# Performance work log

Measured on AMD Instinct MI355X. Metric: run time of the kernel, lower is better.

## Reference

```python
import jax, jax.numpy as jnp
import numpy as np

B, L, C, H, W = 2, 32, 128, 32, 32
R_MIN, R_MAX = 0.8, 0.99


def setup_inputs() -> dict:
    key = jax.random.key(0)
    ks = jax.random.split(key, 12)
    x = jax.random.normal(ks[0], (B, L, C, H, W), jnp.float32)
    # LRU initialization exactly as in the torch module
    u1 = jax.random.uniform(ks[1], (C, H), jnp.float32)
    u2 = jax.random.uniform(ks[2], (C, H), jnp.float32)
    nu_log = jnp.log(-0.5 * jnp.log(u1 * (R_MAX**2 - R_MIN**2) + R_MIN**2))
    theta_log = jnp.log(u2 * 2.0 * jnp.pi)
    abs_lam = jnp.exp(-jnp.exp(nu_log))  # |lambda| = exp(-nu)
    gamma_log = jnp.log(jnp.sqrt(1.0 - abs_lam**2))
    params_log = jnp.concatenate([nu_log, theta_log, gamma_log], axis=0)  # [3C, H]
    s = 0.05
    Wb_re = jax.random.normal(ks[3], (C, C), jnp.float32) * s
    Wb_im = jax.random.normal(ks[4], (C, C), jnp.float32) * s
    bb_re = jax.random.normal(ks[5], (C,), jnp.float32) * s
    bb_im = jax.random.normal(ks[6], (C,), jnp.float32) * s
    Wc_re = jax.random.normal(ks[7], (C, C), jnp.float32) * s
    Wc_im = jax.random.normal(ks[8], (C, C), jnp.float32) * s
    bc_re = jax.random.normal(ks[9], (C,), jnp.float32) * s
    bc_im = jax.random.normal(ks[10], (C,), jnp.float32) * s
    ln_w = jnp.ones((C, H, W), jnp.float32)
    ln_b = jnp.zeros((C, H, W), jnp.float32)
    return dict(x=x, params_log=params_log, Wb_re=Wb_re, Wb_im=Wb_im, bb_re=bb_re,
                bb_im=bb_im, Wc_re=Wc_re, Wc_im=Wc_im, bc_re=bc_re, bc_im=bc_im,
                ln_w=ln_w, ln_b=ln_b)


def reference(x, params_log, Wb_re, Wb_im, bb_re, bb_im, Wc_re, Wc_im, bc_re, bc_im, ln_w, ln_b):
    Cn = x.shape[2]
    nu = jnp.exp(params_log[:Cn])           # [C,H]
    theta = jnpp_exp = jnp.exp(params_log[Cn:2 * Cn])
    gamma = jnp.exp(params_log[2 * Cn:])    # [C,H]
    lam = jnp.exp(-nu + 1j * theta)         # [C,H] complex, |lam|<1

    # FFT2 over spatial dims
    h = jnp.fft.fft2(x.astype(jnp.complex64))  # [B,L,C,H,W]
    # complex 1x1 conv proj_B (CxC GEMM per pixel)
    Wb = (Wb_re + 1j * Wb_im).astype(jnp.complex64)
    bb = (bb_re + 1j * bb_im).astype(jnp.complex64)
    h = jnp.einsum('oc,blchw->blohw', Wb, h) + bb[None, None, :, None, None]
    # gamma gating, broadcast over B,L,W
    h = h * gamma[None, None, :, :, None]

    # linear recurrence y_t = lam * y_{t-1} + h_t (pscan), lam constant in t
    lam_b = lam[None, :, :, None]  # [1,C,H,1] broadcasts over [B,C,H,W]
    def step(carry, ht):
        y = lam_b * carry + ht
        return y, y
    h_t = jnp.moveaxis(h, 1, 0)  # [L,B,C,H,W]
    _, ys = jax.lax.scan(step, jnp.zeros_like(h_t[0]), h_t)
    h = jnp.moveaxis(ys, 0, 1)   # [B,L,C,H,W]
    last_hidden_out = h[:, -1:]

    h = jnp.fft.ifft2(h)
    Wc = (Wc_re + 1j * Wc_im).astype(jnp.complex64)
    bc = (bc_re + 1j * bc_im).astype(jnp.complex64)
    h = jnp.einsum('oc,blchw->blohw', Wc, h) + bc[None, None, :, None, None]
    h = h.real  # real cast, dropout is identity in eval

    # LayerNorm over (C,H,W) jointly
    mean = jnp.mean(h, axis=(2, 3, 4), keepdims=True)
    var = jnp.var(h, axis=(2, 3, 4), keepdims=True)
    h = (h - mean) / jnp.sqrt(var + 1e-5) * ln_w + ln_b
    return h + x, last_hidden_out
```

## Files before the change

kernel.cpp:

```cpp
#include <hip/hip_runtime.h>
#include <cstdint>
#include <cstddef>

#define DEVINL __device__ __forceinline__

static constexpr int Bdim = 2, Ldim = 32, Cdim = 128, Hdim = 32, Wdim = 32;
static constexpr int HW  = Hdim * Wdim;
static constexpr int CHW = Cdim * HW;
static constexpr size_t OUT0_ELEMS = (size_t)Bdim * Ldim * CHW;
static constexpr size_t OUT1_CPLX  = (size_t)Bdim * CHW;

typedef __attribute__((ext_vector_type(8))) short short8v;
typedef __attribute__((ext_vector_type(4))) float f32x4;

DEVINL int bitrev5(int v) {
    return ((v&1)<<4) | ((v&2)<<2) | (v&4) | ((v&8)>>2) | ((v&16)>>4);
}
DEVINL unsigned short f2bf(float v) {
    unsigned u = __float_as_uint(v);
    return (unsigned short)((u + 0x7FFFu + ((u >> 16) & 1u)) >> 16);
}
DEVINL void bfsplit(float v, short& hi, short& lo) {
    unsigned short hb = f2bf(v);
    hi = (short)hb;
    float hf = __uint_as_float(((unsigned)hb) << 16);
    lo = (short)f2bf(v - hf);
}
DEVINL unsigned pack2bf(float2 v) {
    return (unsigned)f2bf(v.x) | ((unsigned)f2bf(v.y) << 16);
}
DEVINL float2 unpack2bf(unsigned u) {
    return make_float2(__uint_as_float(u << 16), __uint_as_float(u & 0xFFFF0000u));
}

template<int INV>
DEVINL void fft32_reg(float2 v[32]) {
    constexpr float TC[16] = { 1.0f, 0.980785280f, 0.923879533f, 0.831469612f,
                               0.707106781f, 0.555570233f, 0.382683432f, 0.195090322f,
                               0.0f, -0.195090322f, -0.382683432f, -0.555570233f,
                              -0.707106781f, -0.831469612f, -0.923879533f, -0.980785280f };
    constexpr float TS[16] = { 0.0f, -0.195090322f, -0.382683432f, -0.555570233f,
                              -0.707106781f, -0.831469612f, -0.923879533f, -0.980785280f,
                              -1.0f, -0.980785280f, -0.923879533f, -0.831469612f,
                              -0.707106781f, -0.555570233f, -0.382683432f, -0.195090322f };
#pragma unroll
    for (int st = 0; st < 5; ++st) {
        const int half = 1 << st;
#pragma unroll
        for (int bf = 0; bf < 16; ++bf) {
            const int g = bf >> st;
            const int j = bf & (half - 1);
            const int i0 = (g << (st+1)) + j;
            const float wr = TC[j << (4-st)];
            const float wi = INV ? -TS[j << (4-st)] : TS[j << (4-st)];
            float2 a0 = v[i0], a1 = v[i0+half];
            float tr = wr*a1.x - wi*a1.y;
            float ti = wr*a1.y + wi*a1.x;
            v[i0]      = make_float2(a0.x+tr, a0.y+ti);
            v[i0+half] = make_float2(a0.x-tr, a0.y-ti);
        }
    }
}

__global__ __launch_bounds__(256) void fft_h_fwd_bf_kernel(const float* __restrict__ x,
                                                           unsigned* __restrict__ Hf) {
    const int gid = blockIdx.x*256 + threadIdx.x;
    const int w = gid & 31;
    const size_t slice = (size_t)(gid >> 5);
    const float* src = x + slice*HW + w;
    float2 v[32];
#pragma unroll
    for (int i = 0; i < 32; ++i)
        v[i] = make_float2(src[(size_t)bitrev5(i)*Wdim], 0.f);
    fft32_reg<0>(v);
    unsigned* dst = Hf + slice*HW + w;
#pragma unroll
    for (int h = 0; h < 32; ++h) dst[(size_t)h*Wdim] = pack2bf(v[h]);
}

__global__ __launch_bounds__(256) void ifft_h_bf_kernel(const unsigned* __restrict__ Sin,
                                                        unsigned* __restrict__ Ysp) {
    const int gid = blockIdx.x*256 + threadIdx.x;
    const int w = gid & 31;
    const size_t slice = (size_t)(gid >> 5);
    const unsigned* src = Sin + slice*HW + w;
    float2 v[32];
#pragma unroll
    for (int i = 0; i < 32; ++i)
        v[i] = unpack2bf(src[(size_t)bitrev5(i)*Wdim]);
    fft32_reg<1>(v);
    const float sc = 1.0f / 32.0f;
    unsigned* dst = Ysp + slice*HW + w;
#pragma unroll
    for (int h = 0; h < 32; ++h)
        dst[(size_t)h*Wdim] = pack2bf(make_float2(v[h].x*sc, v[h].y*sc));
}

__global__ __launch_bounds__(256) void pack_w_kernel(
    const float* __restrict__ Wb_re, const float* __restrict__ Wb_im,
    const float* __restrict__ Wc_re, const float* __restrict__ Wc_im,
    short* __restrict__ Apack)
{
    const int gid = blockIdx.x*256 + threadIdx.x;
    const int a    = gid >> 12;
    const int rem  = gid & 4095;
    const int f    = rem >> 6;
    const int lane = rem & 63;
    const int m  = f >> 3, kc = f & 7;
    const int row = m*16 + (lane & 15);
    const int kbase = kc*32 + ((lane >> 4) << 3);
    short8v hi8, lo8;
#pragma unroll
    for (int j = 0; j < 8; ++j) {
        const int k = kbase + j;
        const int half = k >> 7;
        const int c = k & 127;
        float v;
        if (a == 0)      v = half ? -Wb_im[row*Cdim + c] : Wb_re[row*Cdim + c];
        else if (a == 1) v = half ?  Wb_re[row*Cdim + c] : Wb_im[row*Cdim + c];
        else             v = half ? -Wc_im[row*Cdim + c] : Wc_re[row*Cdim + c];
        short h, l; bfsplit(v, h, l);
        hi8[j] = h; lo8[j] = l;
    }
    const size_t off = (size_t)(f*64 + lane)*8;
    *reinterpret_cast<short8v*>(Apack + (size_t)(2*a)  *32768 + off) = hi8;
    *reinterpret_cast<short8v*>(Apack + (size_t)(2*a+1)*32768 + off) = lo8;
}

template<int MODE>
__global__ __launch_bounds__(256) void mix_mfma3_kernel(
    const unsigned* __restrict__ Yin,
    unsigned* __restrict__ Sout,
    const short* __restrict__ Apack,
    const float* __restrict__ bre, const float* __restrict__ bim,
    const float* __restrict__ pl,
    unsigned short* __restrict__ outr,
    float2* __restrict__ lnpart)
{
    __shared__ short Bs[8][4][64][8];
    const int bx = blockIdx.x;
    const int bl = bx >> 4, tt = bx & 15;
    const int t = threadIdx.x;
    const int wv = t >> 6, lane = t & 63;

    const unsigned* src = Yin + (size_t)bl*CHW + tt*64;
#pragma unroll
    for (int g = 0; g < 4; ++g) {
        const int id = g*256 + t;
        const int hw = id & 63;
        const int co = id >> 6;
        const int kc = co >> 2;
        const int ln = (co & 3)*16 + (hw & 15);
        const int nt4 = hw >> 4;
        unsigned u[8];
#pragma unroll
        for (int j = 0; j < 8; ++j)
            u[j] = src[(size_t)(co*8 + j)*HW + hw];
        unsigned re[4], im[4];
#pragma unroll
        for (int p = 0; p < 4; ++p) {
            re[p] = (u[2*p] & 0xFFFFu) | (u[2*p+1] << 16);
            im[p] = (u[2*p] >> 16) | (u[2*p+1] & 0xFFFF0000u);
        }
        *reinterpret_cast<uint4*>(&Bs[kc][nt4][ln][0])   = make_uint4(re[0], re[1], re[2], re[3]);
        *reinterpret_cast<uint4*>(&Bs[kc+4][nt4][ln][0]) = make_uint4(im[0], im[1], im[2], im[3]);
    }
    __syncthreads();

    f32x4 accRe[2][4];
    f32x4 accIm[2][4];
#pragma unroll
    for (int mi = 0; mi < 2; ++mi)
#pragma unroll
        for (int nt = 0; nt < 4; ++nt) {
            accRe[mi][nt] = (f32x4)(0.0f);
            accIm[mi][nt] = (f32x4)(0.0f);
        }

    const short* Are_hi = Apack + (MODE == 0 ? 0 : 4)*32768;
    const short* Are_lo = Are_hi + 32768;
    const short* Aim_hi = Apack + 2*32768;
    const short* Aim_lo = Aim_hi + 32768;

#pragma unroll 2
    for (int kc = 0; kc < 8; ++kc) {
        short8v bh[4];
#pragma unroll
        for (int nt = 0; nt < 4; ++nt)
            bh[nt] = *reinterpret_cast<const short8v*>(&Bs[kc][nt][lane][0]);
#pragma unroll
        for (int mi = 0; mi < 2; ++mi) {
            const int m = wv*2 + mi;
            const size_t off = (size_t)((m*8 + kc)*64 + lane)*8;
            const short8v arh = *reinterpret_cast<const short8v*>(Are_hi + off);
            const short8v arl = *reinterpret_cast<const short8v*>(Are_lo + off);
#pragma unroll
            for (int nt = 0; nt < 4; ++nt) {
                accRe[mi][nt] = __builtin_amdgcn_mfma_f32_16x16x32_bf16(arh, bh[nt], accRe[mi][nt], 0, 0, 0);
                accRe[mi][nt] = __builtin_amdgcn_mfma_f32_16x16x32_bf16(arl, bh[nt], accRe[mi][nt], 0, 0, 0);
            }
            if (MODE == 0) {
                const short8v aih = *reinterpret_cast<const short8v*>(Aim_hi + off);
                const short8v ail = *reinterpret_cast<const short8v*>(Aim_lo + off);
#pragma unroll
                for (int nt = 0; nt < 4; ++nt) {
                    accIm[mi][nt] = __builtin_amdgcn_mfma_f32_16x16x32_bf16(aih, bh[nt], accIm[mi][nt], 0, 0, 0);
                    accIm[mi][nt] = __builtin_amdgcn_mfma_f32_16x16x32_bf16(ail, bh[nt], accIm[mi][nt], 0, 0, 0);
                }
            }
        }
    }

    const int col   = lane & 15;
    const int rbase = (lane >> 4) * 4;
    float lns = 0.f, lnq = 0.f;
#pragma unroll
    for (int mi = 0; mi < 2; ++mi) {
#pragma unroll
        for (int r = 0; r < 4; ++r) {
            const int o = wv*32 + mi*16 + rbase + r;
            if (MODE == 0) {
                const float br = bre[o], bi = bim[o];
                const float g0 = expf(pl[(2*Cdim + o)*Hdim + 2*tt]);
                const float g1 = expf(pl[(2*Cdim + o)*Hdim + 2*tt + 1]);
#pragma unroll
                for (int nt = 0; nt < 4; ++nt) {
                    const int wcol = nt*16 + col;
                    const float g = (nt < 2) ? g0 : g1;
                    const float bsel = ((wcol & 31) == 0) ? 1.0f : 0.0f;
                    float2 rv;
                    rv.x = (accRe[mi][nt][r] + br*bsel) * g;
                    rv.y = (accIm[mi][nt][r] + bi*bsel) * g;
                    Sout[(size_t)bl*CHW + (size_t)o*HW + tt*64 + wcol] = pack2bf(rv);
                }
            } else {
                const float br = bre[o];
#pragma unroll
                for (int nt = 0; nt < 4; ++nt) {
                    const int wcol = nt*16 + col;
                    const float v = accRe[mi][nt][r] + br;
                    outr[(size_t)bl*CHW + (size_t)o*HW + tt*64 + wcol] = f2bf(v);
                    lns += v; lnq += v*v;
                }
            }
        }
    }
    if (MODE == 1) {
#pragma unroll
        for (int off = 32; off > 0; off >>= 1) {
            lns += __shfl_down(lns, off);
            lnq += __shfl_down(lnq, off);
        }
        __shared__ float2 red[4];
        if (lane == 0) red[wv] = make_float2(lns, lnq);
        __syncthreads();
        if (t == 0) {
            float2 a = red[0], b2 = red[1], c2 = red[2], d = red[3];
            lnpart[bx] = make_float2(a.x + b2.x + c2.x + d.x, a.y + b2.y + c2.y + d.y);
        }
    }
}

template<int CPLX>
__global__ __launch_bounds__(256) void scan_fftw_kernel(
    unsigned* __restrict__ Hf2, const float* __restrict__ pl, float* __restrict__ out1)
{
    const int idx = blockIdx.x*256 + threadIdx.x;
    const int b   = idx >> 17;
    const int chw = idx & (CHW - 1);
    const int c   = chw >> 10;
    const int h   = (chw >> 5) & 31;
    const float nu = expf(pl[c*Hdim + h]);
    const float th = expf(pl[(Cdim + c)*Hdim + h]);
    const float rr = expf(-nu);
    const float lr = rr * cosf(th);
    const float li = rr * sinf(th);
    float2 y = make_float2(0.f, 0.f);
    const size_t basei = (size_t)b * Ldim * CHW + chw;
#pragma unroll 4
    for (int l = 0; l < Ldim; ++l) {
        float2 hv = unpack2bf(Hf2[basei + (size_t)l*CHW]);
        float yr = fmaf(lr, y.x, fmaf(-li, y.y, hv.x));
        float yi = fmaf(lr, y.y, fmaf( li, y.x, hv.y));
        y = make_float2(yr, yi);
        Hf2[basei + (size_t)l*CHW] = pack2bf(y);
    }
    const int a = threadIdx.x & 31;
    float2 v;
    v.x = __shfl(y.x, bitrev5(a), 32);
    v.y = __shfl(y.y, bitrev5(a), 32);
#pragma unroll
    for (int st = 0; st < 5; ++st) {
        const int half = 1 << st;
        const int j = a & (half - 1);
        const float ang = -6.283185307179586f * (float)(j << (4 - st)) / 32.0f;
        float wi, wr;
        __sincosf(ang, &wi, &wr);
        float2 p;
        p.x = __shfl_xor(v.x, half, 32);
        p.y = __shfl_xor(v.y, half, 32);
        const bool top = (a & half) == 0;
        const float2 a1 = top ? p : v;
        const float2 a0 = top ? v : p;
        const float tr = wr*a1.x - wi*a1.y;
        const float ti = wr*a1.y + wi*a1.x;
        v.x = top ? a0.x + tr : a0.x - tr;
        v.y = top ? a0.y + ti : a0.y - ti;
    }
    const size_t row = (size_t)(idx >> 5);
    if (CPLX) {
        reinterpret_cast<float2*>(out1)[row*32 + a] = v;
    } else {
        out1[row*32 + a] = v.x;
    }
}

__global__ __launch_bounds__(64) void ln_finish_kernel(const float2* __restrict__ lnpart,
                                                       float2* __restrict__ stats) {
    const int bl = blockIdx.x;
    const int t = threadIdx.x;
    float s = 0.f, sq = 0.f;
    if (t < 16) { float2 v = lnpart[bl*16 + t]; s = v.x; sq = v.y; }
#pragma unroll
    for (int off = 8; off > 0; off >>= 1) {
        s  += __shfl_down(s, off);
        sq += __shfl_down(sq, off);
    }
    if (t == 0) {
        const float invN = 1.0f / (float)CHW;
        float mean = s * invN;
        float var  = sq * invN - mean*mean;
        stats[bl] = make_float2(mean, rsqrtf(var + 1e-5f));
    }
}

__global__ __launch_bounds__(256) void ln_apply_kernel(
    float* __restrict__ out0, const unsigned short* __restrict__ hpre,
    const float* __restrict__ x,
    const float* __restrict__ lnw, const float* __restrict__ lnb,
    const float2* __restrict__ stats)
{
    const int idx4 = blockIdx.x*256 + threadIdx.x;
    const int i = idx4 * 4;
    const int bl = i >> 17;
    const int chw4 = (i & (CHW - 1)) >> 2;
    const float2 st = stats[bl];
    const uint2 hu = reinterpret_cast<const uint2*>(hpre)[idx4];
    float4 h;
    h.x = __uint_as_float(hu.x << 16);
    h.y = __uint_as_float(hu.x & 0xFFFF0000u);
    h.z = __uint_as_float(hu.y << 16);
    h.w = __uint_as_float(hu.y & 0xFFFF0000u);
    float4 xv = reinterpret_cast<const float4*>(x)[idx4];
    float4 w  = reinterpret_cast<const float4*>(lnw)[chw4];
    float4 bb = reinterpret_cast<const float4*>(lnb)[chw4];
    const float m = st.x, rs = st.y;
    float4 r;
    r.x = fmaf((h.x - m)*rs, w.x, bb.x) + xv.x;
    r.y = fmaf((h.y - m)*rs, w.y, bb.y) + xv.y;
    r.z = fmaf((h.z - m)*rs, w.z, bb.z) + xv.z;
    r.w = fmaf((h.w - m)*rs, w.w, bb.w) + xv.w;
    reinterpret_cast<float4*>(out0)[idx4] = r;
}

extern "C" void kernel_launch(void* const* d_in, const int* in_sizes, int n_in,
                              void* d_out, int out_size, void* d_ws, size_t ws_size,
                              hipStream_t stream)
{
    const float* x     = (const float*)d_in[0];
    const float* pl    = (const float*)d_in[1];
    const float* Wb_re = (const float*)d_in[2];
    const float* Wb_im = (const float*)d_in[3];
    const float* bb_re = (const float*)d_in[4];
    const float* bb_im = (const float*)d_in[5];
    const float* Wc_re = (const float*)d_in[6];
    const float* Wc_im = (const float*)d_in[7];
    const float* bc_re = (const float*)d_in[8];
    const float* bc_im = (const float*)d_in[9];
    const float* ln_w  = (const float*)d_in[10];
    const float* ln_b  = (const float*)d_in[11];
    (void)bc_im;

    float* out0 = (float*)d_out;
    float* out1 = out0 + OUT0_ELEMS;

    char* ws = (char*)d_ws;
    unsigned*       bufA    = (unsigned*)       ws;
    unsigned*       bufB    = (unsigned*)       (ws + 33554432);
    unsigned short* out0pre = (unsigned short*) (ws + 67108864);
    short*          Apack   = (short*)          (ws + 83886080);
    float2*         lnpart  = (float2*)         (ws + 84279296);
    float2*         stats   = (float2*)         (ws + 84287488);

    const bool interleaved = ((size_t)out_size >= OUT0_ELEMS + 2*OUT1_CPLX);

    pack_w_kernel<<<48, 256, 0, stream>>>(Wb_re, Wb_im, Wc_re, Wc_im, Apack);
    fft_h_fwd_bf_kernel<<<1024, 256, 0, stream>>>(x, bufA);
    mix_mfma3_kernel<0><<<1024, 256, 0, stream>>>(bufA, bufB, Apack, bb_re, bb_im, pl, nullptr, nullptr);
    if (interleaved)
        scan_fftw_kernel<1><<<1024, 256, 0, stream>>>(bufB, pl, out1);
    else
        scan_fftw_kernel<0><<<1024, 256, 0, stream>>>(bufB, pl, out1);
    ifft_h_bf_kernel<<<1024, 256, 0, stream>>>(bufB, bufA);
    mix_mfma3_kernel<1><<<1024, 256, 0, stream>>>(bufA, nullptr, Apack, bc_re, bc_im, pl, out0pre, lnpart);
    ln_finish_kernel<<<64, 64, 0, stream>>>(lnpart, stats);
    ln_apply_kernel<<<8192, 256, 0, stream>>>(out0, out0pre, x, ln_w, ln_b, stats);
}
```

Baseline: 103.1 us.

## Apply channel mix before FFT on real input to halve first GEMM

The forward path now uses linearity to commute the complex channel projection with the H-axis FFT. The real input x is multiplied by Wb_re and Wb_im in the spatial domain with K=128 instead of the previous K=256 complex-expanded GEMM. The FFT over H then runs on the mixed complex data, with the bias and gamma gating applied afterwards using a precomputed gamma table. This cuts MFMA work in the first mix and removes expf calls from that epilogue. The cost is a new bf16 rounding of x before the GEMM, in addition to the rounding of the FFT intermediate.

```diff
diff --git a/kernel.cpp b/kernel.cpp
--- a/kernel.cpp
+++ b/kernel.cpp
@@ -62,20 +62,169 @@
     }
 }
 
-__global__ __launch_bounds__(256) void fft_h_fwd_bf_kernel(const float* __restrict__ x,
-                                                           unsigned* __restrict__ Hf) {
+__global__ __launch_bounds__(256) void pack_w_kernel(
+    const float* __restrict__ Wb_re, const float* __restrict__ Wb_im,
+    const float* __restrict__ Wc_re, const float* __restrict__ Wc_im,
+    const float* __restrict__ pl,
+    short* __restrict__ Apack, float* __restrict__ gamma_tab)
+{
+    const int gid = blockIdx.x*256 + threadIdx.x;
+    if (gid < 4096) {
+        const int a2   = gid >> 11;
+        const int rem  = gid & 2047;
+        const int f    = rem >> 6;
+        const int lane = rem & 63;
+        const int m  = f >> 2, kc = f & 3;
+        const int row = m*16 + (lane & 15);
+        const int kbase = kc*32 + ((lane >> 4) << 3);
+        short8v hi8, lo8;
+#pragma unroll
+        for (int j = 0; j < 8; ++j) {
+            const int c = kbase + j;
+            const float v = a2 ? Wb_im[row*Cdim + c] : Wb_re[row*Cdim + c];
+            short h, l; bfsplit(v, h, l);
+            hi8[j] = h; lo8[j] = l;
+        }
+        const size_t off = (size_t)(f*64 + lane)*8;
+        const size_t base = (size_t)a2 * 32768;
+        *reinterpret_cast<short8v*>(Apack + base + off)         = hi8;
+        *reinterpret_cast<short8v*>(Apack + base + 16384 + off) = lo8;
+    } else if (gid < 8192) {
+        const int rem  = gid - 4096;
+        const int f    = rem >> 6;
+        const int lane = rem & 63;
+        const int m  = f >> 3, kc = f & 7;
+        const int row = m*16 + (lane & 15);
+        const int kbase = kc*32 + ((lane >> 4) << 3);
+        short8v hi8, lo8;
+#pragma unroll
+        for (int j = 0; j < 8; ++j) {
+            const int k = kbase + j;
+            const int half = k >> 7;
+            const int c = k & 127;
+            const float v = half ? -Wc_im[row*Cdim + c] : Wc_re[row*Cdim + c];
+            short h, l; bfsplit(v, h, l);
+            hi8[j] = h; lo8[j] = l;
+        }
+        const size_t off = (size_t)(f*64 + lane)*8;
+        *reinterpret_cast<short8v*>(Apack + 65536 + off)         = hi8;
+        *reinterpret_cast<short8v*>(Apack + 65536 + 32768 + off) = lo8;
+    } else {
+        const int idx = gid - 8192;
+        const int c = idx >> 5, hf = idx & 31;
+        gamma_tab[idx] = expf(pl[(2*Cdim + c)*Hdim + hf]);
+    }
+}
+
+__global__ __launch_bounds__(256) void mix0_spatial_kernel(
+    const float* __restrict__ x,
+    unsigned* __restrict__ Sout,
+    const short* __restrict__ Apack)
+{
+    __shared__ short Bs[4][4][64][8];
+    const int bx = blockIdx.x;
+    const int bl = bx >> 4, tt = bx & 15;
+    const int t = threadIdx.x;
+    const int wv = t >> 6, lane = t & 63;
+
+    const float* src = x + (size_t)bl*CHW + tt*64;
+#pragma unroll
+    for (int g = 0; g < 4; ++g) {
+        const int id = g*256 + t;
+        const int hw = id & 63;
+        const int co = id >> 6;
+        const int kc = co >> 2;
+        const int ln = (co & 3)*16 + (hw & 15);
+        const int nt4 = hw >> 4;
+        short8v b8;
+#pragma unroll
+        for (int j = 0; j < 8; ++j)
+            b8[j] = (short)f2bf(src[(size_t)(co*8 + j)*HW + hw]);
+        *reinterpret_cast<short8v*>(&Bs[kc][nt4][ln][0]) = b8;
+    }
+    __syncthreads();
+
+    f32x4 accRe[2][4];
+    f32x4 accIm[2][4];
+#pragma unroll
+    for (int mi = 0; mi < 2; ++mi)
+#pragma unroll
+        for (int nt = 0; nt < 4; ++nt) {
+            accRe[mi][nt] = (f32x4)(0.0f);
+            accIm[mi][nt] = (f32x4)(0.0f);
+        }
+
+    const short* Are_hi = Apack;
+    const short* Are_lo = Apack + 16384;
+    const short* Aim_hi = Apack + 32768;
+    const short* Aim_lo = Apack + 49152;
+
+#pragma unroll 2
+    for (int kc = 0; kc < 4; ++kc) {
+        short8v bh[4];
+#pragma unroll
+        for (int nt = 0; nt < 4; ++nt)
+            bh[nt] = *reinterpret_cast<const short8v*>(&Bs[kc][nt][lane][0]);
+#pragma unroll
+        for (int mi = 0; mi < 2; ++mi) {
+            const int m = wv*2 + mi;
+            const size_t off = (size_t)((m*4 + kc)*64 + lane)*8;
+            const short8v arh = *reinterpret_cast<const short8v*>(Are_hi + off);
+            const short8v arl = *reinterpret_cast<const short8v*>(Are_lo + off);
+            const short8v aih = *reinterpret_cast<const short8v*>(Aim_hi + off);
+            const short8v ail = *reinterpret_cast<const short8v*>(Aim_lo + off);
+#pragma unroll
+            for (int nt = 0; nt < 4; ++nt) {
+                accRe[mi][nt] = __builtin_amdgcn_mfma_f32_16x16x32_bf16(arh, bh[nt], accRe[mi][nt], 0, 0, 0);
+                accRe[mi][nt] = __builtin_amdgcn_mfma_f32_16x16x32_bf16(arl, bh[nt], accRe[mi][nt], 0, 0, 0);
+                accIm[mi][nt] = __builtin_amdgcn_mfma_f32_16x16x32_bf16(aih, bh[nt], accIm[mi][nt], 0, 0, 0);
+                accIm[mi][nt] = __builtin_amdgcn_mfma_f32_16x16x32_bf16(ail, bh[nt], accIm[mi][nt], 0, 0, 0);
+            }
+        }
+    }
+
+    const int col   = lane & 15;
+    const int rbase = (lane >> 4) * 4;
+#pragma unroll
+    for (int mi = 0; mi < 2; ++mi) {
+#pragma unroll
+        for (int r = 0; r < 4; ++r) {
+            const int o = wv*32 + mi*16 + rbase + r;
+#pragma unroll
+            for (int nt = 0; nt < 4; ++nt) {
+                const int wcol = nt*16 + col;
+                float2 rv = make_float2(accRe[mi][nt][r], accIm[mi][nt][r]);
+                Sout[(size_t)bl*CHW + (size_t)o*HW + tt*64 + wcol] = pack2bf(rv);
+            }
+        }
+    }
+}
+
+__global__ __launch_bounds__(256) void fft_gamma_kernel(
+    const unsigned* __restrict__ Hsp,
+    unsigned* __restrict__ Hfq,
+    const float* __restrict__ gamma_tab,
+    const float* __restrict__ bb_re, const float* __restrict__ bb_im)
+{
     const int gid = blockIdx.x*256 + threadIdx.x;
     const int w = gid & 31;
     const size_t slice = (size_t)(gid >> 5);
-    const float* src = x + slice*HW + w;
+    const int c = (int)(slice & 127);
+    const unsigned* src = Hsp + slice*HW + w;
     float2 v[32];
 #pragma unroll
     for (int i = 0; i < 32; ++i)
-        v[i] = make_float2(src[(size_t)bitrev5(i)*Wdim], 0.f);
+        v[i] = unpack2bf(src[(size_t)bitrev5(i)*Wdim]);
     fft32_reg<0>(v);
-    unsigned* dst = Hf + slice*HW + w;
-#pragma unroll
-    for (int h = 0; h < 32; ++h) dst[(size_t)h*Wdim] = pack2bf(v[h]);
+    const float br = (w == 0) ? bb_re[c] : 0.0f;
+    const float bi = (w == 0) ? bb_im[c] : 0.0f;
+    const float* gt = gamma_tab + c*32;
+    unsigned* dst = Hfq + slice*HW + w;
+#pragma unroll
+    for (int hf = 0; hf < 32; ++hf) {
+        const float g = gt[hf];
+        dst[(size_t)hf*Wdim] = pack2bf(make_float2((v[hf].x + br)*g, (v[hf].y + bi)*g));
+    }
 }
 
 __global__ __launch_bounds__(256) void ifft_h_bf_kernel(const unsigned* __restrict__ Sin,
@@ -96,44 +245,10 @@
         dst[(size_t)h*Wdim] = pack2bf(make_float2(v[h].x*sc, v[h].y*sc));
 }
 
-__global__ __launch_bounds__(256) void pack_w_kernel(
-    const float* __restrict__ Wb_re, const float* __restrict__ Wb_im,
-    const float* __restrict__ Wc_re, const float* __restrict__ Wc_im,
-    short* __restrict__ Apack)
-{
-    const int gid = blockIdx.x*256 + threadIdx.x;
-    const int a    = gid >> 12;
-    const int rem  = gid & 4095;
-    const int f    = rem >> 6;
-    const int lane = rem & 63;
-    const int m  = f >> 3, kc = f & 7;
-    const int row = m*16 + (lane & 15);
-    const int kbase = kc*32 + ((lane >> 4) << 3);
-    short8v hi8, lo8;
-#pragma unroll
-    for (int j = 0; j < 8; ++j) {
-        const int k = kbase + j;
-        const int half = k >> 7;
-        const int c = k & 127;
-        float v;
-        if (a == 0)      v = half ? -Wb_im[row*Cdim + c] : Wb_re[row*Cdim + c];
-        else if (a == 1) v = half ?  Wb_re[row*Cdim + c] : Wb_im[row*Cdim + c];
-        else             v = half ? -Wc_im[row*Cdim + c] : Wc_re[row*Cdim + c];
-        short h, l; bfsplit(v, h, l);
-        hi8[j] = h; lo8[j] = l;
-    }
-    const size_t off = (size_t)(f*64 + lane)*8;
-    *reinterpret_cast<short8v*>(Apack + (size_t)(2*a)  *32768 + off) = hi8;
-    *reinterpret_cast<short8v*>(Apack + (size_t)(2*a+1)*32768 + off) = lo8;
-}
-
-template<int MODE>
-__global__ __launch_bounds__(256) void mix_mfma3_kernel(
+__global__ __launch_bounds__(256) void mix1_kernel(
     const unsigned* __restrict__ Yin,
-    unsigned* __restrict__ Sout,
     const short* __restrict__ Apack,
-    const float* __restrict__ bre, const float* __restrict__ bim,
-    const float* __restrict__ pl,
+    const float* __restrict__ bre,
     unsigned short* __restrict__ outr,
     float2* __restrict__ lnpart)
 {
@@ -167,20 +282,14 @@
     }
     __syncthreads();
 
-    f32x4 accRe[2][4];
-    f32x4 accIm[2][4];
+    f32x4 acc[2][4];
 #pragma unroll
     for (int mi = 0; mi < 2; ++mi)
 #pragma unroll
-        for (int nt = 0; nt < 4; ++nt) {
-            accRe[mi][nt] = (f32x4)(0.0f);
-            accIm[mi][nt] = (f32x4)(0.0f);
-        }
-
-    const short* Are_hi = Apack + (MODE == 0 ? 0 : 4)*32768;
-    const short* Are_lo = Are_hi + 32768;
-    const short* Aim_hi = Apack + 2*32768;
-    const short* Aim_lo = Aim_hi + 32768;
+        for (int nt = 0; nt < 4; ++nt) acc[mi][nt] = (f32x4)(0.0f);
+
+    const short* A_hi = Apack + 65536;
+    const short* A_lo = Apack + 65536 + 32768;
 
 #pragma unroll 2
     for (int kc = 0; kc < 8; ++kc) {
@@ -192,21 +301,12 @@
         for (int mi = 0; mi < 2; ++mi) {
             const int m = wv*2 + mi;
             const size_t off = (size_t)((m*8 + kc)*64 + lane)*8;
-            const short8v arh = *reinterpret_cast<const short8v*>(Are_hi + off);
-            const short8v arl = *reinterpret_cast<const short8v*>(Are_lo + off);
+            const short8v arh = *reinterpret_cast<const short8v*>(A_hi + off);
+            const short8v arl = *reinterpret_cast<const short8v*>(A_lo + off);
 #pragma unroll
             for (int nt = 0; nt < 4; ++nt) {
-                accRe[mi][nt] = __builtin_amdgcn_mfma_f32_16x16x32_bf16(arh, bh[nt], accRe[mi][nt], 0, 0, 0);
-                accRe[mi][nt] = __builtin_amdgcn_mfma_f32_16x16x32_bf16(arl, bh[nt], accRe[mi][nt], 0, 0, 0);
-            }
-            if (MODE == 0) {
-                const short8v aih = *reinterpret_cast<const short8v*>(Aim_hi + off);
-                const short8v ail = *reinterpret_cast<const short8v*>(Aim_lo + off);
-#pragma unroll
-                for (int nt = 0; nt < 4; ++nt) {
-                    accIm[mi][nt] = __builtin_amdgcn_mfma_f32_16x16x32_bf16(aih, bh[nt], accIm[mi][nt], 0, 0, 0);
-                    accIm[mi][nt] = __builtin_amdgcn_mfma_f32_16x16x32_bf16(ail, bh[nt], accIm[mi][nt], 0, 0, 0);
-                }
+                acc[mi][nt] = __builtin_amdgcn_mfma_f32_16x16x32_bf16(arh, bh[nt], acc[mi][nt], 0, 0, 0);
+                acc[mi][nt] = __builtin_amdgcn_mfma_f32_16x16x32_bf16(arl, bh[nt], acc[mi][nt], 0, 0, 0);
             }
         }
     }
@@ -219,45 +319,27 @@
 #pragma unroll
         for (int r = 0; r < 4; ++r) {
             const int o = wv*32 + mi*16 + rbase + r;
-            if (MODE == 0) {
-                const float br = bre[o], bi = bim[o];
-                const float g0 = expf(pl[(2*Cdim + o)*Hdim + 2*tt]);
-                const float g1 = expf(pl[(2*Cdim + o)*Hdim + 2*tt + 1]);
-#pragma unroll
-                for (int nt = 0; nt < 4; ++nt) {
-                    const int wcol = nt*16 + col;
-                    const float g = (nt < 2) ? g0 : g1;
-                    const float bsel = ((wcol & 31) == 0) ? 1.0f : 0.0f;
-                    float2 rv;
-                    rv.x = (accRe[mi][nt][r] + br*bsel) * g;
-                    rv.y = (accIm[mi][nt][r] + bi*bsel) * g;
-                    Sout[(size_t)bl*CHW + (size_t)o*HW + tt*64 + wcol] = pack2bf(rv);
-                }
-            } else {
-                const float br = bre[o];
-#pragma unroll
-                for (int nt = 0; nt < 4; ++nt) {
-                    const int wcol = nt*16 + col;
-                    const float v = accRe[mi][nt][r] + br;
-                    outr[(size_t)bl*CHW + (size_t)o*HW + tt*64 + wcol] = f2bf(v);
-                    lns += v; lnq += v*v;
-                }
+            const float br = bre[o];
+#pragma unroll
+            for (int nt = 0; nt < 4; ++nt) {
+                const int wcol = nt*16 + col;
+                const float v = acc[mi][nt][r] + br;
+                outr[(size_t)bl*CHW + (size_t)o*HW + tt*64 + wcol] = f2bf(v);
+                lns += v; lnq += v*v;
             }
         }
     }
-    if (MODE == 1) {
-#pragma unroll
-        for (int off = 32; off > 0; off >>= 1) {
-            lns += __shfl_down(lns, off);
-            lnq += __shfl_down(lnq, off);
-        }
-        __shared__ float2 red[4];
-        if (lane == 0) red[wv] = make_float2(lns, lnq);
-        __syncthreads();
-        if (t == 0) {
-            float2 a = red[0], b2 = red[1], c2 = red[2], d = red[3];
-            lnpart[bx] = make_float2(a.x + b2.x + c2.x + d.x, a.y + b2.y + c2.y + d.y);
-        }
+#pragma unroll
+    for (int off = 32; off > 0; off >>= 1) {
+        lns += __shfl_down(lns, off);
+        lnq += __shfl_down(lnq, off);
+    }
+    __shared__ float2 red[4];
+    if (lane == 0) red[wv] = make_float2(lns, lnq);
+    __syncthreads();
+    if (t == 0) {
+        float2 a = red[0], b2 = red[1], c2 = red[2], d = red[3];
+        lnpart[bx] = make_float2(a.x + b2.x + c2.x + d.x, a.y + b2.y + c2.y + d.y);
     }
 }
 
@@ -389,20 +471,21 @@
     unsigned*       bufB    = (unsigned*)       (ws + 33554432);
     unsigned short* out0pre = (unsigned short*) (ws + 67108864);
     short*          Apack   = (short*)          (ws + 83886080);
-    float2*         lnpart  = (float2*)         (ws + 84279296);
-    float2*         stats   = (float2*)         (ws + 84287488);
+    float*          gtab    = (float*)          (ws + 84148224);
+    float2*         lnpart  = (float2*)         (ws + 84164608);
+    float2*         stats   = (float2*)         (ws + 84172800);
 
     const bool interleaved = ((size_t)out_size >= OUT0_ELEMS + 2*OUT1_CPLX);
 
-    pack_w_kernel<<<48, 256, 0, stream>>>(Wb_re, Wb_im, Wc_re, Wc_im, Apack);
-    fft_h_fwd_bf_kernel<<<1024, 256, 0, stream>>>(x, bufA);
-    mix_mfma3_kernel<0><<<1024, 256, 0, stream>>>(bufA, bufB, Apack, bb_re, bb_im, pl, nullptr, nullptr);
+    pack_w_kernel<<<48, 256, 0, stream>>>(Wb_re, Wb_im, Wc_re, Wc_im, pl, Apack, gtab);
+    mix0_spatial_kernel<<<1024, 256, 0, stream>>>(x, bufA, Apack);
+    fft_gamma_kernel<<<1024, 256, 0, stream>>>(bufA, bufB, gtab, bb_re, bb_im);
     if (interleaved)
         scan_fftw_kernel<1><<<1024, 256, 0, stream>>>(bufB, pl, out1);
     else
         scan_fftw_kernel<0><<<1024, 256, 0, stream>>>(bufB, pl, out1);
     ifft_h_bf_kernel<<<1024, 256, 0, stream>>>(bufB, bufA);
-    mix_mfma3_kernel<1><<<1024, 256, 0, stream>>>(bufA, nullptr, Apack, bc_re, bc_im, pl, out0pre, lnpart);
+    mix1_kernel<<<1024, 256, 0, stream>>>(bufA, Apack, bc_re, out0pre, lnpart);
     ln_finish_kernel<<<64, 64, 0, stream>>>(lnpart, stats);
     ln_apply_kernel<<<8192, 256, 0, stream>>>(out0, out0pre, x, ln_w, ln_b, stats);
 }
```

Measured after the change: 97.65 us. 5.3% less time.
